# Optimization experiments

Measured on AMD Instinct MI355X. Metric: run time of the kernel, lower is better.

The kernel has to match this reference:

```python
import jax, jax.numpy as jnp
import numpy as np

TEMPERATURE = 0.1
BATCH_SIZE = 64
EPS = 1e-8  # torch.nn.CosineSimilarity eps
NEG_INF = -1e30

B, C, D = 64, 16, 512  # batch, children per sample, feature dim


def setup_inputs() -> dict:
    key = jax.random.key(0)
    k1, k2, k3, k4 = jax.random.split(key, 4)
    children_is = jax.random.normal(k1, (B, C, D), dtype=jnp.float32)
    children_js = jax.random.normal(k2, (B, C, D), dtype=jnp.float32)
    partnet_ids = jnp.arange(B, dtype=jnp.int64 if jax.config.jax_enable_x64 else jnp.int32)
    neg_idx_j = jax.random.randint(k3, (B, B, C), 0, C)  # negatives drawn from children_js
    neg_idx_k = jax.random.randint(k4, (B, B, C), 0, C)  # negatives drawn from children_is
    return {
        "children_is": children_is,
        "children_js": children_js,
        "partnet_ids": partnet_ids,
        "neg_idx_j": neg_idx_j,
        "neg_idx_k": neg_idx_k,
    }


def _safe_norm(x, axis=-1):
    return jnp.maximum(jnp.sqrt(jnp.sum(x * x, axis=axis)), EPS)


def _ntxent(ci, cj, pids, nj, nk):
    b = ci.shape[0]
    fi = ci.reshape(b, -1)  # [B, L] flattened anchors
    fj = cj.reshape(b, -1)  # [B, L] flattened positives
    norm_i = _safe_norm(fi)

    # positive: cos(flat(children_i), flat(children_j[i])) / T
    pos = jnp.sum(fi * fj, axis=-1) / (norm_i * _safe_norm(fj))  # [B]

    src = jnp.arange(b)[None, :, None]  # broadcast source-sample index
    # gathered negatives: g*[i, j] = children_*[j, neg_idx[i, j]] flattened -> [B, B, L]
    gj = cj[src, nj].reshape(b, b, -1)
    gk = ci[src, nk].reshape(b, b, -1)

    sim_j = jnp.einsum('il,ijl->ij', fi, gj) / (norm_i[:, None] * _safe_norm(gj))
    sim_k = jnp.einsum('il,ijl->ij', fi, gk) / (norm_i[:, None] * _safe_norm(gk))

    # negative pair valid iff j != i and partnet ids differ
    eye = jnp.arange(b)
    mask = (eye[None, :] != eye[:, None]) & (pids[None, :] != pids[:, None])  # [B, B]

    logits = jnp.concatenate(
        [pos[:, None],
         jnp.where(mask, sim_j, NEG_INF),
         jnp.where(mask, sim_k, NEG_INF)], axis=1) / TEMPERATURE  # [B, 1+2B]

    # CrossEntropy with label 0, reduction='sum' over the batch of anchors
    loss = jnp.sum(-logits[:, 0] + jax.scipy.special.logsumexp(logits, axis=1))
    return loss / (2.0 * BATCH_SIZE)


def reference(children_is, children_js, partnet_ids, neg_idx_j, neg_idx_k):
    return _ntxent(children_is, children_js, partnet_ids, neg_idx_j, neg_idx_k)
```

## Files before the change

### kernel.cpp

```cpp
#include <hip/hip_runtime.h>
#include <math.h>

#define BB 64
#define CC 16
#define DD 512
#define LL 8192
#define EPSV 1e-8f
#define INVT 10.0f
#define NEGINF_T (-1e31f)

#define OFF_CIB 0
#define OFF_CJB (1u << 20)
#define OFF_D   (2u << 20)
#define OFF_N2I (10u << 20)
#define OFF_N2J ((10u << 20) + 4096u)
#define OFF_POS ((10u << 20) + 8192u)

typedef short bf16x8 __attribute__((ext_vector_type(8)));
typedef float f32x4  __attribute__((ext_vector_type(4)));

__device__ __forceinline__ float dot4(float4 a, float4 b) {
    return a.x * b.x + a.y * b.y + a.z * b.z + a.w * b.w;
}
__device__ __forceinline__ float wave_reduce(float v) {
    #pragma unroll
    for (int off = 32; off; off >>= 1) v += __shfl_down(v, off);
    return v;
}
__device__ __forceinline__ unsigned short f2bf(float f) {
    union { float f; unsigned u; } x; x.f = f;
    return (unsigned short)((x.u + 0x7fffu + ((x.u >> 16) & 1u)) >> 16);
}

__global__ __launch_bounds__(256) void ntx_prep(const float* __restrict__ ci,
                                                const float* __restrict__ cj,
                                                char* __restrict__ ws,
                                                float* __restrict__ out) {
    const int b = blockIdx.x, tid = threadIdx.x;
    const int wave = tid >> 6, lane = tid & 63;
    __shared__ float red[4];

    if (b < 512) {
        const int r  = b * 4 + wave;
        const int rr = r & 1023;
        const bool is_i = (r < 1024);
        const float* src = is_i ? ci : cj;
        unsigned short* dst = (unsigned short*)(ws + (is_i ? OFF_CIB : OFF_CJB));
        float4 v1 = ((const float4*)(src + rr * DD))[lane];
        float4 v2 = ((const float4*)(src + rr * DD))[64 + lane];
        float acc = wave_reduce(dot4(v1, v1) + dot4(v2, v2));
        if (lane == 0) ((float*)(ws + (is_i ? OFF_N2I : OFF_N2J)))[rr] = acc;
        ushort4 h1 = { f2bf(v1.x), f2bf(v1.y), f2bf(v1.z), f2bf(v1.w) };
        ushort4 h2 = { f2bf(v2.x), f2bf(v2.y), f2bf(v2.z), f2bf(v2.w) };
        ((ushort4*)(dst + rr * DD))[lane]      = h1;
        ((ushort4*)(dst + rr * DD))[64 + lane] = h2;
    } else {
        const int i = b - 512;
        if (b == 512 && tid == 0) out[0] = 0.f;
        const float4* fi = (const float4*)(ci + i * LL);
        const float4* fj = (const float4*)(cj + i * LL);
        float acc = 0.f;
        #pragma unroll
        for (int it = 0; it < 8; ++it) acc += dot4(fi[tid + 256 * it], fj[tid + 256 * it]);
        acc = wave_reduce(acc);
        if (lane == 0) red[wave] = acc;
        __syncthreads();
        if (tid == 0) ((float*)(ws + OFF_POS))[i] = red[0] + red[1] + red[2] + red[3];
    }
}

__global__ __launch_bounds__(256) void ntx_gemm(const char* __restrict__ ws_c,
                                                float* __restrict__ D) {
    const int bm = blockIdx.x;
    const int bn = blockIdx.y;
    const int tid = threadIdx.x;
    const int wave = tid >> 6, lane = tid & 63;
    const int wm = wave >> 1, wn = wave & 1;
    const int quad = lane >> 4, lr = lane & 15;

    const short* A = (const short*)(ws_c + OFF_CIB);
    const bool isj = (bn < 16);
    const short* B = (const short*)(ws_c + (isj ? OFF_CJB : OFF_CIB));
    const int row0 = bm * 64 + wm * 32;
    const int nrow0 = (isj ? bn : bn - 16) * 64 + wn * 32;

    f32x4 acc[2][2] = {};
    const int ka = quad * 8;

    #pragma unroll 4
    for (int kk = 0; kk < 16; ++kk) {
        const int k = kk * 32 + ka;
        bf16x8 a0 = *(const bf16x8*)(A + (row0 + lr) * DD + k);
        bf16x8 a1 = *(const bf16x8*)(A + (row0 + 16 + lr) * DD + k);
        bf16x8 b0 = *(const bf16x8*)(B + (nrow0 + lr) * DD + k);
        bf16x8 b1 = *(const bf16x8*)(B + (nrow0 + 16 + lr) * DD + k);
        acc[0][0] = __builtin_amdgcn_mfma_f32_16x16x32_bf16(a0, b0, acc[0][0], 0, 0, 0);
        acc[0][1] = __builtin_amdgcn_mfma_f32_16x16x32_bf16(a0, b1, acc[0][1], 0, 0, 0);
        acc[1][0] = __builtin_amdgcn_mfma_f32_16x16x32_bf16(a1, b0, acc[1][0], 0, 0, 0);
        acc[1][1] = __builtin_amdgcn_mfma_f32_16x16x32_bf16(a1, b1, acc[1][1], 0, 0, 0);
    }

    const int gcol0 = bn * 64 + wn * 32;
    #pragma unroll
    for (int a = 0; a < 2; ++a) {
        #pragma unroll
        for (int b = 0; b < 2; ++b) {
            const int row = row0 + a * 16 + quad * 4;
            const int col = gcol0 + b * 16 + lr;
            #pragma unroll
            for (int r = 0; r < 4; ++r)
                D[(row + r) * 2048 + col] = acc[a][b][r];
        }
    }
}

__global__ __launch_bounds__(64) void ntx_final(const int* __restrict__ pids,
                                                const int* __restrict__ nj,
                                                const int* __restrict__ nk,
                                                const char* __restrict__ ws_c,
                                                float* __restrict__ out) {
    const int i = blockIdx.x, j = threadIdx.x;
    const float* D   = (const float*)(ws_c + OFF_D);
    const float* n2i = (const float*)(ws_c + OFF_N2I);
    const float* n2j = (const float*)(ws_c + OFF_N2J);
    const float* pos = (const float*)(ws_c + OFF_POS);

    float si = 0.f, sjf = 0.f;
    #pragma unroll
    for (int c = 0; c < CC; ++c) { si += n2i[i * CC + c]; sjf += n2j[i * CC + c]; }
    const float ni = fmaxf(sqrtf(si), EPSV);
    const float l0 = pos[i] / (ni * fmaxf(sqrtf(sjf), EPSV)) * INVT;

    int4 njv[4], nkv[4];
    #pragma unroll
    for (int t = 0; t < 4; ++t) {
        njv[t] = ((const int4*)(nj + (i * BB + j) * CC))[t];
        nkv[t] = ((const int4*)(nk + (i * BB + j) * CC))[t];
    }
    float gj = 0.f, gk = 0.f, dj = 0.f, dk = 0.f;
    #pragma unroll
    for (int t = 0; t < 4; ++t) {
        const int aj[4] = { njv[t].x, njv[t].y, njv[t].z, njv[t].w };
        const int ak[4] = { nkv[t].x, nkv[t].y, nkv[t].z, nkv[t].w };
        #pragma unroll
        for (int u = 0; u < 4; ++u) {
            const int c = t * 4 + u;
            gj += n2j[j * CC + aj[u]];
            gk += n2i[j * CC + ak[u]];
            dj += D[(i * CC + c) * 2048 + j * CC + aj[u]];
            dk += D[(i * CC + c) * 2048 + 1024 + j * CC + ak[u]];
        }
    }

    const bool valid = (j != i) && (pids[j] != pids[i]);
    float lj = NEGINF_T, lk = NEGINF_T;
    if (valid) {
        const float inv = INVT / ni;
        lj = dj / fmaxf(sqrtf(gj), EPSV) * inv;
        lk = dk / fmaxf(sqrtf(gk), EPSV) * inv;
    }

    float m = fmaxf(lj, lk);
    #pragma unroll
    for (int off = 32; off; off >>= 1) m = fmaxf(m, __shfl_xor(m, off));
    m = fmaxf(m, l0);

    float s = __expf(lj - m) + __expf(lk - m);
    s = wave_reduce(s);
    if (j == 0) {
        s += __expf(l0 - m);
        const float loss_i = -l0 + m + __logf(s);
        atomicAdd(out, loss_i * (1.0f / (2.0f * BB)));
    }
}

extern "C" void kernel_launch(void* const* d_in, const int* in_sizes, int n_in,
                              void* d_out, int out_size, void* d_ws, size_t ws_size,
                              hipStream_t stream) {
    const float* ci  = (const float*)d_in[0];
    const float* cj  = (const float*)d_in[1];
    const int*  pids = (const int*) d_in[2];
    const int*  nj   = (const int*) d_in[3];
    const int*  nk   = (const int*) d_in[4];
    char*  ws  = (char*)d_ws;
    float* out = (float*)d_out;

    ntx_prep<<<576, 256, 0, stream>>>(ci, cj, ws, out);
    ntx_gemm<<<dim3(16, 32), 256, 0, stream>>>(ws, (float*)(ws + OFF_D));
    ntx_final<<<BB, 64, 0, stream>>>(pids, nj, nk, ws, out);
}
```

Before: 88.33 us.

## Fuse gather-reduction into GEMM strip kernel, drop the full similarity matrix

Replaces the full 1024x2048 similarity GEMM, which wrote a 8MB matrix to global memory, with a per-anchor strip kernel. Each block computes the 16x512 tile for one anchor sample in LDS and immediately gathers the indexed diagonal entries and norms into compact per-(i,j) sums. This removes the large global write and the scattered reads in the final kernel. In exchange each block does a long serial K loop with eight MFMAs per step and fewer blocks, and it uses 32KB of LDS per block.

```diff
diff --git a/kernel.cpp b/kernel.cpp
--- a/kernel.cpp
+++ b/kernel.cpp
@@ -9,12 +9,16 @@
 #define INVT 10.0f
 #define NEGINF_T (-1e31f)
 
-#define OFF_CIB 0
+#define OFF_CIB 0u
 #define OFF_CJB (1u << 20)
-#define OFF_D   (2u << 20)
-#define OFF_N2I (10u << 20)
-#define OFF_N2J ((10u << 20) + 4096u)
-#define OFF_POS ((10u << 20) + 8192u)
+#define BASE2   (2u << 20)
+#define OFF_N2I (BASE2)
+#define OFF_N2J (BASE2 + 4096u)
+#define OFF_POS (BASE2 + 8192u)
+#define OFF_DJ  (BASE2 + 12288u)
+#define OFF_DK  (BASE2 + 12288u + 16384u)
+#define OFF_GJ  (BASE2 + 12288u + 32768u)
+#define OFF_GK  (BASE2 + 12288u + 49152u)
 
 typedef short bf16x8 __attribute__((ext_vector_type(8)));
 typedef float f32x4  __attribute__((ext_vector_type(4)));
@@ -69,58 +73,64 @@
     }
 }
 
-__global__ __launch_bounds__(256) void ntx_gemm(const char* __restrict__ ws_c,
-                                                float* __restrict__ D) {
-    const int bm = blockIdx.x;
-    const int bn = blockIdx.y;
-    const int tid = threadIdx.x;
+__global__ __launch_bounds__(256) void ntx_strip(const int* __restrict__ nj,
+                                                 const int* __restrict__ nk,
+                                                 char* __restrict__ ws) {
+    const int b = blockIdx.x;
+    const int i = b >> 2, q = b & 3;
+    const int side = q >> 1, jh = q & 1;
+    const int tid  = threadIdx.x;
     const int wave = tid >> 6, lane = tid & 63;
-    const int wm = wave >> 1, wn = wave & 1;
     const int quad = lane >> 4, lr = lane & 15;
 
-    const short* A = (const short*)(ws_c + OFF_CIB);
-    const bool isj = (bn < 16);
-    const short* B = (const short*)(ws_c + (isj ? OFF_CJB : OFF_CIB));
-    const int row0 = bm * 64 + wm * 32;
-    const int nrow0 = (isj ? bn : bn - 16) * 64 + wn * 32;
+    __shared__ float sS[16][512];
 
-    f32x4 acc[2][2] = {};
-    const int ka = quad * 8;
+    const short* A  = (const short*)(ws + OFF_CIB) + i * CC * DD;
+    const short* Bm = (const short*)(ws + (side ? OFF_CIB : OFF_CJB)) + jh * 512 * DD;
 
-    #pragma unroll 4
+    f32x4 acc[8] = {};
+    #pragma unroll
     for (int kk = 0; kk < 16; ++kk) {
-        const int k = kk * 32 + ka;
-        bf16x8 a0 = *(const bf16x8*)(A + (row0 + lr) * DD + k);
-        bf16x8 a1 = *(const bf16x8*)(A + (row0 + 16 + lr) * DD + k);
-        bf16x8 b0 = *(const bf16x8*)(B + (nrow0 + lr) * DD + k);
-        bf16x8 b1 = *(const bf16x8*)(B + (nrow0 + 16 + lr) * DD + k);
-        acc[0][0] = __builtin_amdgcn_mfma_f32_16x16x32_bf16(a0, b0, acc[0][0], 0, 0, 0);
-        acc[0][1] = __builtin_amdgcn_mfma_f32_16x16x32_bf16(a0, b1, acc[0][1], 0, 0, 0);
-        acc[1][0] = __builtin_amdgcn_mfma_f32_16x16x32_bf16(a1, b0, acc[1][0], 0, 0, 0);
-        acc[1][1] = __builtin_amdgcn_mfma_f32_16x16x32_bf16(a1, b1, acc[1][1], 0, 0, 0);
+        const int k = kk * 32 + quad * 8;
+        bf16x8 av = *(const bf16x8*)(A + lr * DD + k);
+        #pragma unroll
+        for (int tt = 0; tt < 8; ++tt) {
+            const int row = (wave * 8 + tt) * 16 + lr;
+            bf16x8 bv = *(const bf16x8*)(Bm + row * DD + k);
+            acc[tt] = __builtin_amdgcn_mfma_f32_16x16x32_bf16(av, bv, acc[tt], 0, 0, 0);
+        }
     }
+    #pragma unroll
+    for (int tt = 0; tt < 8; ++tt) {
+        const int t = wave * 8 + tt;
+        #pragma unroll
+        for (int r = 0; r < 4; ++r)
+            sS[quad * 4 + r][t * 16 + lr] = acc[tt][r];
+    }
+    __syncthreads();
 
-    const int gcol0 = bn * 64 + wn * 32;
-    #pragma unroll
-    for (int a = 0; a < 2; ++a) {
-        #pragma unroll
-        for (int b = 0; b < 2; ++b) {
-            const int row = row0 + a * 16 + quad * 4;
-            const int col = gcol0 + b * 16 + lr;
-            #pragma unroll
-            for (int r = 0; r < 4; ++r)
-                D[(row + r) * 2048 + col] = acc[a][b][r];
-        }
+    const int jj = tid >> 3;
+    const int g  = tid & 7;
+    const int j  = jh * 32 + jj;
+    const int* idxp = (side ? nk : nj) + (i * BB + j) * CC;
+    const float* n2 = (const float*)(ws + (side ? OFF_N2I : OFF_N2J)) + j * CC;
+    const int c0 = g * 2;
+    const int x0 = idxp[c0], x1 = idxp[c0 + 1];
+    float d  = sS[c0][jj * 16 + x0] + sS[c0 + 1][jj * 16 + x1];
+    float gn = n2[x0] + n2[x1];
+    d += __shfl_down(d, 4);  gn += __shfl_down(gn, 4);
+    d += __shfl_down(d, 2);  gn += __shfl_down(gn, 2);
+    d += __shfl_down(d, 1);  gn += __shfl_down(gn, 1);
+    if (g == 0) {
+        ((float*)(ws + (side ? OFF_DK : OFF_DJ)))[i * BB + j] = d;
+        ((float*)(ws + (side ? OFF_GK : OFF_GJ)))[i * BB + j] = gn;
     }
 }
 
 __global__ __launch_bounds__(64) void ntx_final(const int* __restrict__ pids,
-                                                const int* __restrict__ nj,
-                                                const int* __restrict__ nk,
                                                 const char* __restrict__ ws_c,
                                                 float* __restrict__ out) {
     const int i = blockIdx.x, j = threadIdx.x;
-    const float* D   = (const float*)(ws_c + OFF_D);
     const float* n2i = (const float*)(ws_c + OFF_N2I);
     const float* n2j = (const float*)(ws_c + OFF_N2J);
     const float* pos = (const float*)(ws_c + OFF_POS);
@@ -131,26 +141,10 @@
     const float ni = fmaxf(sqrtf(si), EPSV);
     const float l0 = pos[i] / (ni * fmaxf(sqrtf(sjf), EPSV)) * INVT;
 
-    int4 njv[4], nkv[4];
-    #pragma unroll
-    for (int t = 0; t < 4; ++t) {
-        njv[t] = ((const int4*)(nj + (i * BB + j) * CC))[t];
-        nkv[t] = ((const int4*)(nk + (i * BB + j) * CC))[t];
-    }
-    float gj = 0.f, gk = 0.f, dj = 0.f, dk = 0.f;
-    #pragma unroll
-    for (int t = 0; t < 4; ++t) {
-        const int aj[4] = { njv[t].x, njv[t].y, njv[t].z, njv[t].w };
-        const int ak[4] = { nkv[t].x, nkv[t].y, nkv[t].z, nkv[t].w };
-        #pragma unroll
-        for (int u = 0; u < 4; ++u) {
-            const int c = t * 4 + u;
-            gj += n2j[j * CC + aj[u]];
-            gk += n2i[j * CC + ak[u]];
-            dj += D[(i * CC + c) * 2048 + j * CC + aj[u]];
-            dk += D[(i * CC + c) * 2048 + 1024 + j * CC + ak[u]];
-        }
-    }
+    const float dj = ((const float*)(ws_c + OFF_DJ))[i * BB + j];
+    const float dk = ((const float*)(ws_c + OFF_DK))[i * BB + j];
+    const float gj = ((const float*)(ws_c + OFF_GJ))[i * BB + j];
+    const float gk = ((const float*)(ws_c + OFF_GK))[i * BB + j];
 
     const bool valid = (j != i) && (pids[j] != pids[i]);
     float lj = NEGINF_T, lk = NEGINF_T;
@@ -186,6 +180,6 @@
     float* out = (float*)d_out;
 
     ntx_prep<<<576, 256, 0, stream>>>(ci, cj, ws, out);
-    ntx_gemm<<<dim3(16, 32), 256, 0, stream>>>(ws, (float*)(ws + OFF_D));
-    ntx_final<<<BB, 64, 0, stream>>>(pids, nj, nk, ws, out);
+    ntx_strip<<<256, 256, 0, stream>>>(nj, nk, ws);
+    ntx_final<<<BB, 64, 0, stream>>>(pids, ws, out);
 }
```

New measurement: 86.47 us. 1.02x faster.
